# Kernel optimization log

Measured on AMD Instinct MI355X. Metric: run time of the kernel, lower is better.

Reference implementation:

```python
import jax, jax.numpy as jnp
import numpy as np

N, E, B = 50000, 800000, 64     # nodes, edges, graphs
IN, H = 3, 64                   # in_channels, hidden_channels
NDEF = 6
EPS = 1e-5                      # BatchNorm eps


def setup_inputs() -> dict:
    key = jax.random.key(0)
    ks = jax.random.split(key, 32)

    def lin(k, fi, fo):
        kw, kb = jax.random.split(k)
        s = 1.0 / np.sqrt(fi)
        W = jax.random.uniform(kw, (fi, fo), jnp.float32, -s, s)
        b = jax.random.uniform(kb, (fo,), jnp.float32, -s, s)
        return W, b

    inp = {}
    inp["x"] = jax.random.normal(ks[0], (N, IN), jnp.float32)
    inp["edge_index"] = jax.random.randint(ks[1], (2, E), 0, N, jnp.int64)
    inp["batch"] = jnp.sort(jax.random.randint(ks[2], (N,), 0, B, jnp.int64))

    inp["W1"], inp["b1"] = lin(ks[3], IN, H)
    inp["W2"], inp["b2"] = lin(ks[4], H, H)
    inp["W3"], inp["b3"] = lin(ks[5], H, H)
    for i, kk in zip((1, 2, 3), (ks[6], ks[7], ks[8])):
        kg, kb2 = jax.random.split(kk)
        inp[f"bn{i}_g"] = 1.0 + 0.1 * jax.random.normal(kg, (H,), jnp.float32)
        inp[f"bn{i}_b"] = 0.1 * jax.random.normal(kb2, (H,), jnp.float32)
        inp[f"bn{i}_m"] = jnp.zeros((H,), jnp.float32)
        inp[f"bn{i}_v"] = jnp.ones((H,), jnp.float32)

    inp["th_W1"], inp["th_b1"] = lin(ks[9], H, H // 2)
    inp["th_W2"], inp["th_b2"] = lin(ks[10], H // 2, NDEF)
    inp["lh_W1"], inp["lh_b1"] = lin(ks[11], H, H // 2)
    inp["lh_W2"], inp["lh_b2"] = lin(ks[12], H // 2, 2)
    inp["sh_W1"], inp["sh_b1"] = lin(ks[13], H, H // 4)
    inp["sh_W2"], inp["sh_b2"] = lin(ks[14], H // 4, 1)
    return inp


def reference(x, edge_index, batch,
              W1, b1, W2, b2, W3, b3,
              bn1_g, bn1_b, bn1_m, bn1_v,
              bn2_g, bn2_b, bn2_m, bn2_v,
              bn3_g, bn3_b, bn3_m, bn3_v,
              th_W1, th_b1, th_W2, th_b2,
              lh_W1, lh_b1, lh_W2, lh_b2,
              sh_W1, sh_b1, sh_W2, sh_b2):
    src, dst = edge_index[0], edge_index[1]
    # GCN symmetric normalization with self-loops: deg counts in-edges + self
    deg = jax.ops.segment_sum(jnp.ones((E,), x.dtype), dst, num_segments=N) + 1.0
    dis = jax.lax.rsqrt(deg)                 # deg^{-1/2}  [N]
    enorm = (dis[src] * dis[dst])[:, None]   # per-edge norm
    snorm = (dis * dis)[:, None]             # self-loop norm

    def gcn(h, W, b):
        m = h @ W  # [N, H]
        agg = jax.ops.segment_sum(m[src] * enorm, dst, num_segments=N) + m * snorm
        return agg + b

    def bn(h, g, beta, mu, var):
        return (h - mu) * jax.lax.rsqrt(var + EPS) * g + beta

    h = jax.nn.relu(bn(gcn(x, W1, b1), bn1_g, bn1_b, bn1_m, bn1_v))
    h = jax.nn.relu(bn(gcn(h, W2, b2), bn2_g, bn2_b, bn2_m, bn2_v))
    h = jax.nn.relu(bn(gcn(h, W3, b3), bn3_g, bn3_b, bn3_m, bn3_v))

    # global_mean_pool over graphs
    cnt = jax.ops.segment_sum(jnp.ones((N,), h.dtype), batch, num_segments=B)
    gemb = jax.ops.segment_sum(h, batch, num_segments=B) / jnp.maximum(cnt, 1.0)[:, None]

    type_logits = jax.nn.relu(gemb @ th_W1 + th_b1) @ th_W2 + th_b2
    location = jax.nn.sigmoid(jax.nn.relu(gemb @ lh_W1 + lh_b1) @ lh_W2 + lh_b2)
    severity = jax.nn.sigmoid(jax.nn.relu(gemb @ sh_W1 + sh_b1) @ sh_W2 + sh_b2)
    return (type_logits, location, severity)
```

## Files before the change

### kernel.cpp

```cpp
#include <hip/hip_runtime.h>
#include <hip/hip_bf16.h>
#include <math.h>

#define HH 64
#define EPS 1e-5f
#define STAGE_CAP 12288
#define NBLK_SCAT 192
#define PER_LANE 3

__device__ __forceinline__ int lower_bound_i(const int* a, int n, int key) {
    int lo = 0, hi = n;
    while (lo < hi) { int mid = (lo + hi) >> 1; if (a[mid] < key) lo = mid + 1; else hi = mid; }
    return lo;
}

__device__ __forceinline__ unsigned short f2bf(float f) {
    unsigned int u = __float_as_uint(f);
    unsigned int r = (u + 0x7FFFu + ((u >> 16) & 1u)) >> 16;
    return (unsigned short)r;
}
__device__ __forceinline__ float bf2f(unsigned short b) {
    return __uint_as_float(((unsigned int)b) << 16);
}

__global__ void init_kernel(float* gsum, int NG) {
    int t = blockIdx.x * blockDim.x + threadIdx.x;
    if (t < NG) gsum[t] = 0.f;
}

__global__ __launch_bounds__(256) void hist_kernel(const int* __restrict__ dst,
        int* __restrict__ blockhist, int E, int chunk) {
    __shared__ int hist[256];
    int tid = threadIdx.x, blk = blockIdx.x;
    hist[tid] = 0;
    __syncthreads();
    int s = blk * chunk, e = s + chunk; if (e > E) e = E;
    for (int i = s + tid; i < e; i += 256) atomicAdd(&hist[dst[i] >> 8], 1);
    __syncthreads();
    blockhist[blk * 256 + tid] = hist[tid];
}

__global__ __launch_bounds__(256) void bucketscan_kernel(const int* __restrict__ blockhist,
        int* __restrict__ bucketbase, int NB, int E) {
    __shared__ int wsum2[4];
    int tid = threadIdx.x, lane = tid & 63, wid = tid >> 6;
    int s = 0;
    if (tid < NB) {
        for (int i = 0; i < NBLK_SCAT; ++i) s += blockhist[i * 256 + tid];
    }
    int incl = s;
    #pragma unroll
    for (int off = 1; off < 64; off <<= 1) {
        int n = __shfl_up(incl, off);
        if (lane >= off) incl += n;
    }
    if (lane == 63) wsum2[wid] = incl;
    __syncthreads();
    int wbase = 0;
    #pragma unroll
    for (int k = 0; k < 4; ++k) if (k < wid) wbase += wsum2[k];
    if (tid < NB) bucketbase[tid] = wbase + incl - s;
    if (tid == 0) bucketbase[NB] = E;
}

__global__ __launch_bounds__(64) void offsets_kernel(const int* __restrict__ bucketbase,
        int* __restrict__ blockhist, int NB) {
    int b = blockIdx.x;
    int lane = threadIdx.x;
    int v[PER_LANE];
    int base = lane * PER_LANE;
    int s = 0;
    #pragma unroll
    for (int k = 0; k < PER_LANE; ++k) {
        int i = base + k;
        v[k] = (i < NBLK_SCAT) ? blockhist[i * 256 + b] : 0;
        s += v[k];
    }
    int incl = s;
    #pragma unroll
    for (int off = 1; off < 64; off <<= 1) {
        int n = __shfl_up(incl, off);
        if (lane >= off) incl += n;
    }
    int excl = incl - s + bucketbase[b];
    #pragma unroll
    for (int k = 0; k < PER_LANE; ++k) {
        int i = base + k;
        if (i < NBLK_SCAT) { blockhist[i * 256 + b] = excl; excl += v[k]; }
    }
}

__global__ __launch_bounds__(256) void scatterA_kernel(const int* __restrict__ src,
        const int* __restrict__ dst, const int* __restrict__ blockhist,
        int* __restrict__ buf, int E, int chunk) {
    __shared__ int lcur[256];
    int tid = threadIdx.x, blk = blockIdx.x;
    lcur[tid] = blockhist[blk * 256 + tid];
    __syncthreads();
    int s = blk * chunk, e = s + chunk; if (e > E) e = E;
    for (int i = s + tid; i < e; i += 256) {
        int d = dst[i];
        int b = d >> 8;
        int p = atomicAdd(&lcur[b], 1);
        buf[p] = ((d & 255) << 24) | src[i];
    }
}

__global__ __launch_bounds__(256) void bucket_to_csr_kernel(const int* __restrict__ buf,
        const int* __restrict__ bucketbase, int* __restrict__ rowstart,
        float* __restrict__ dis, int* __restrict__ csr, int N, int E) {
    __shared__ int ldeg[256];
    __shared__ int cur[256];
    __shared__ int wsum2[4];
    __shared__ int stage[STAGE_CAP];
    int b = blockIdx.x;
    int nodeStart = b << 8;
    int nodeEnd = nodeStart + 256; if (nodeEnd > N) nodeEnd = N;
    int nloc = nodeEnd - nodeStart;
    int base = bucketbase[b];
    int nE = bucketbase[b + 1] - base;
    int tid = threadIdx.x;
    int lane = tid & 63, wid = tid >> 6;
    ldeg[tid] = 0;
    __syncthreads();
    for (int i = tid; i < nE; i += 256)
        atomicAdd(&ldeg[((unsigned)buf[base + i]) >> 24], 1);
    __syncthreads();
    int d = ldeg[tid];
    int incl = d;
    #pragma unroll
    for (int off = 1; off < 64; off <<= 1) {
        int n = __shfl_up(incl, off);
        if (lane >= off) incl += n;
    }
    if (lane == 63) wsum2[wid] = incl;
    __syncthreads();
    int wbase = 0;
    #pragma unroll
    for (int k = 0; k < 4; ++k) if (k < wid) wbase += wsum2[k];
    int excl = wbase + incl - d;
    cur[tid] = excl;
    if (tid < nloc) {
        rowstart[nodeStart + tid] = base + excl;
        dis[nodeStart + tid] = rsqrtf((float)d + 1.0f);
    }
    if (b == 0 && tid == 0) rowstart[N] = E;
    __syncthreads();
    if (nE <= STAGE_CAP) {
        for (int i = tid; i < nE; i += 256) {
            int u = buf[base + i];
            int l = ((unsigned)u) >> 24;
            int p = atomicAdd(&cur[l], 1);
            stage[p] = u & 0xFFFFFF;
        }
        __syncthreads();
        for (int i = tid; i < nE; i += 256) csr[base + i] = stage[i];
    } else {
        for (int i = tid; i < nE; i += 256) {
            int u = buf[base + i];
            int l = ((unsigned)u) >> 24;
            int p = atomicAdd(&cur[l], 1);
            csr[base + p] = u & 0xFFFFFF;
        }
    }
}

__global__ void mt1_kernel(const float* __restrict__ x, const float* __restrict__ W1,
                           const float* __restrict__ dis, unsigned short* __restrict__ mt, int N) {
    int t = blockIdx.x * blockDim.x + threadIdx.x;
    if (t < N * HH) {
        int v = t >> 6, c = t & 63;
        float m = x[v * 3 + 0] * W1[0 * HH + c]
                + x[v * 3 + 1] * W1[1 * HH + c]
                + x[v * 3 + 2] * W1[2 * HH + c];
        mt[t] = f2bf(m * dis[v]);
    }
}

__global__ __launch_bounds__(256) void gemm_scale_kernel(const float* __restrict__ h,
        const float* __restrict__ W, const float* __restrict__ dis,
        unsigned short* __restrict__ mt, int N) {
    __shared__ unsigned int wsp[HH * 34];
    __shared__ unsigned int hs2[64 * 34];
    int tid = threadIdx.x;
    int lane = tid & 63, wid = tid >> 6;

    {
        int c = tid & 63;
        for (int k2 = tid >> 6; k2 < 32; k2 += 4) {
            float a = W[(2 * k2) * HH + c];
            float b = W[(2 * k2 + 1) * HH + c];
            wsp[c * 34 + k2] = (unsigned)f2bf(a) | ((unsigned)f2bf(b) << 16);
        }
    }
    int v0 = blockIdx.x * 64;
    int nv = N - v0; if (nv > 64) nv = 64;
    for (int idx = tid; idx < 64 * 32; idx += 256) {
        int n = idx >> 5, k2 = idx & 31;
        int vsrc = v0 + ((n < nv) ? n : 0);
        float a = h[(size_t)vsrc * HH + 2 * k2];
        float b = h[(size_t)vsrc * HH + 2 * k2 + 1];
        hs2[n * 34 + k2] = (unsigned)f2bf(a) | ((unsigned)f2bf(b) << 16);
    }
    __syncthreads();

    for (int n = wid * 16; n < wid * 16 + 16; ++n) {
        int vg = v0 + n;
        if (n >= nv) break;
        float acc = 0.f;
        #pragma unroll 4
        for (int k2g = 0; k2g < 16; ++k2g) {
            uint2 wv = *(const uint2*)&wsp[lane * 34 + 2 * k2g];
            uint2 hv = *(const uint2*)&hs2[n * 34 + 2 * k2g];
            acc = fmaf(__uint_as_float(hv.x << 16),         __uint_as_float(wv.x << 16),         acc);
            acc = fmaf(__uint_as_float(hv.x & 0xFFFF0000u), __uint_as_float(wv.x & 0xFFFF0000u), acc);
            acc = fmaf(__uint_as_float(hv.y << 16),         __uint_as_float(wv.y << 16),         acc);
            acc = fmaf(__uint_as_float(hv.y & 0xFFFF0000u), __uint_as_float(wv.y & 0xFFFF0000u), acc);
        }
        mt[(size_t)vg * HH + lane] = f2bf(acc * dis[vg]);
    }
}

__global__ __launch_bounds__(256) void gather_bn_kernel(const unsigned short* __restrict__ mt,
        const int* __restrict__ rowstart, const int* __restrict__ csr_src,
        const float* __restrict__ dis, const float* __restrict__ bias,
        const float* __restrict__ gam, const float* __restrict__ beta,
        const float* __restrict__ mu, const float* __restrict__ var,
        float* __restrict__ hout, int N) {
    int lane = threadIdx.x & 63, wid = threadIdx.x >> 6;
    int v = blockIdx.x * 4 + wid;
    if (v >= N) return;
    int start = rowstart[v], end = rowstart[v + 1];
    float acc = bf2f(mt[v * HH + lane]);
    for (int base = start; base < end; base += 64) {
        int idx = (base + lane < end) ? csr_src[base + lane] : 0;
        int cnt = end - base; if (cnt > 64) cnt = 64;
        int j = 0;
        for (; j + 15 < cnt; j += 16) {
            int s0 = __shfl(idx, j),      s1 = __shfl(idx, j + 1);
            int s2 = __shfl(idx, j + 2),  s3 = __shfl(idx, j + 3);
            int s4 = __shfl(idx, j + 4),  s5 = __shfl(idx, j + 5);
            int s6 = __shfl(idx, j + 6),  s7 = __shfl(idx, j + 7);
            int s8 = __shfl(idx, j + 8),  s9 = __shfl(idx, j + 9);
            int sa = __shfl(idx, j + 10), sb = __shfl(idx, j + 11);
            int sc = __shfl(idx, j + 12), sd = __shfl(idx, j + 13);
            int se = __shfl(idx, j + 14), sf = __shfl(idx, j + 15);
            float v0 = bf2f(mt[s0 * HH + lane]);
            float v1 = bf2f(mt[s1 * HH + lane]);
            float v2 = bf2f(mt[s2 * HH + lane]);
            float v3 = bf2f(mt[s3 * HH + lane]);
            float v4 = bf2f(mt[s4 * HH + lane]);
            float v5 = bf2f(mt[s5 * HH + lane]);
            float v6 = bf2f(mt[s6 * HH + lane]);
            float v7 = bf2f(mt[s7 * HH + lane]);
            float v8 = bf2f(mt[s8 * HH + lane]);
            float v9 = bf2f(mt[s9 * HH + lane]);
            float va = bf2f(mt[sa * HH + lane]);
            float vb = bf2f(mt[sb * HH + lane]);
            float vc = bf2f(mt[sc * HH + lane]);
            float vd = bf2f(mt[sd * HH + lane]);
            float ve = bf2f(mt[se * HH + lane]);
            float vf = bf2f(mt[sf * HH + lane]);
            acc += v0; acc += v1; acc += v2; acc += v3;
            acc += v4; acc += v5; acc += v6; acc += v7;
            acc += v8; acc += v9; acc += va; acc += vb;
            acc += vc; acc += vd; acc += ve; acc += vf;
        }
        for (; j + 7 < cnt; j += 8) {
            int s0 = __shfl(idx, j),     s1 = __shfl(idx, j + 1);
            int s2 = __shfl(idx, j + 2), s3 = __shfl(idx, j + 3);
            int s4 = __shfl(idx, j + 4), s5 = __shfl(idx, j + 5);
            int s6 = __shfl(idx, j + 6), s7 = __shfl(idx, j + 7);
            float v0 = bf2f(mt[s0 * HH + lane]);
            float v1 = bf2f(mt[s1 * HH + lane]);
            float v2 = bf2f(mt[s2 * HH + lane]);
            float v3 = bf2f(mt[s3 * HH + lane]);
            float v4 = bf2f(mt[s4 * HH + lane]);
            float v5 = bf2f(mt[s5 * HH + lane]);
            float v6 = bf2f(mt[s6 * HH + lane]);
            float v7 = bf2f(mt[s7 * HH + lane]);
            acc += v0; acc += v1; acc += v2; acc += v3;
            acc += v4; acc += v5; acc += v6; acc += v7;
        }
        for (; j < cnt; ++j) acc += bf2f(mt[__shfl(idx, j) * HH + lane]);
    }
    float val = acc * dis[v] + bias[lane];
    val = (val - mu[lane]) * rsqrtf(var[lane] + EPS) * gam[lane] + beta[lane];
    hout[v * HH + lane] = fmaxf(val, 0.f);
}

__global__ __launch_bounds__(256) void pool_partial_kernel(const float* __restrict__ h,
        const int* __restrict__ batch, float* __restrict__ gsum, int N, int chunk) {
    int lane = threadIdx.x & 63, wid = threadIdx.x >> 6;
    int w = blockIdx.x * 4 + wid;
    int start = w * chunk;
    int end = start + chunk; if (end > N) end = N;
    if (start >= end) return;
    int g = batch[start];
    float acc = 0.f;
    for (int i = start; i < end; ++i) {
        int gi = batch[i];
        if (gi != g) {
            atomicAdd(&gsum[g * HH + lane], acc);
            acc = 0.f; g = gi;
        }
        acc += h[i * HH + lane];
    }
    atomicAdd(&gsum[g * HH + lane], acc);
}

__global__ __launch_bounds__(64) void heads_kernel(const float* __restrict__ gsum,
        const int* __restrict__ batch, int N,
        const float* __restrict__ thW1, const float* __restrict__ thb1,
        const float* __restrict__ thW2, const float* __restrict__ thb2,
        const float* __restrict__ lhW1, const float* __restrict__ lhb1,
        const float* __restrict__ lhW2, const float* __restrict__ lhb2,
        const float* __restrict__ shW1, const float* __restrict__ shb1,
        const float* __restrict__ shW2, const float* __restrict__ shb2,
        float* __restrict__ out, int B) {
    int g = blockIdx.x, t = threadIdx.x;
    __shared__ float ge[HH];
    __shared__ float hT[32], hL[32], hS[16];
    int lo = lower_bound_i(batch, N, g);
    int hi = lower_bound_i(batch, N, g + 1);
    float cnt = (float)(hi - lo);
    ge[t] = gsum[g * HH + t] / fmaxf(cnt, 1.0f);
    __syncthreads();
    if (t < 32) {
        float a = thb1[t];
        for (int k = 0; k < HH; ++k) a += ge[k] * thW1[k * 32 + t];
        hT[t] = fmaxf(a, 0.f);
    } else {
        int j = t - 32;
        float a = lhb1[j];
        for (int k = 0; k < HH; ++k) a += ge[k] * lhW1[k * 32 + j];
        hL[j] = fmaxf(a, 0.f);
    }
    __syncthreads();
    if (t < 16) {
        float a = shb1[t];
        for (int k = 0; k < HH; ++k) a += ge[k] * shW1[k * 16 + t];
        hS[t] = fmaxf(a, 0.f);
    }
    __syncthreads();
    if (t < 6) {
        float a = thb2[t];
        for (int j = 0; j < 32; ++j) a += hT[j] * thW2[j * 6 + t];
        out[g * 6 + t] = a;
    } else if (t >= 8 && t < 10) {
        int o = t - 8;
        float a = lhb2[o];
        for (int j = 0; j < 32; ++j) a += hL[j] * lhW2[j * 2 + o];
        out[B * 6 + g * 2 + o] = 1.f / (1.f + expf(-a));
    } else if (t == 12) {
        float a = shb2[0];
        for (int j = 0; j < 16; ++j) a += hS[j] * shW2[j];
        out[B * 8 + g] = 1.f / (1.f + expf(-a));
    }
}

extern "C" void kernel_launch(void* const* d_in, const int* in_sizes, int n_in,
                              void* d_out, int out_size, void* d_ws, size_t ws_size,
                              hipStream_t stream) {
    const float* x   = (const float*)d_in[0];
    const int*   ei  = (const int*)d_in[1];
    const int*   bat = (const int*)d_in[2];
    const float* W1 = (const float*)d_in[3];  const float* b1 = (const float*)d_in[4];
    const float* W2 = (const float*)d_in[5];  const float* b2 = (const float*)d_in[6];
    const float* W3 = (const float*)d_in[7];  const float* b3 = (const float*)d_in[8];
    const float* bn1g = (const float*)d_in[9];  const float* bn1b = (const float*)d_in[10];
    const float* bn1m = (const float*)d_in[11]; const float* bn1v = (const float*)d_in[12];
    const float* bn2g = (const float*)d_in[13]; const float* bn2b = (const float*)d_in[14];
    const float* bn2m = (const float*)d_in[15]; const float* bn2v = (const float*)d_in[16];
    const float* bn3g = (const float*)d_in[17]; const float* bn3b = (const float*)d_in[18];
    const float* bn3m = (const float*)d_in[19]; const float* bn3v = (const float*)d_in[20];
    const float* thW1 = (const float*)d_in[21]; const float* thb1 = (const float*)d_in[22];
    const float* thW2 = (const float*)d_in[23]; const float* thb2 = (const float*)d_in[24];
    const float* lhW1 = (const float*)d_in[25]; const float* lhb1 = (const float*)d_in[26];
    const float* lhW2 = (const float*)d_in[27]; const float* lhb2 = (const float*)d_in[28];
    const float* shW1 = (const float*)d_in[29]; const float* shb1 = (const float*)d_in[30];
    const float* shW2 = (const float*)d_in[31]; const float* shb2 = (const float*)d_in[32];
    float* out = (float*)d_out;

    const int N = in_sizes[0] / 3;
    const int E = in_sizes[1] / 2;
    const int B = out_size / 9;
    const int NB = (N + 255) >> 8;
    const int* esrc = ei;
    const int* edst = ei + E;

    char* w = (char*)d_ws;
    size_t off = 0;
    auto alloc = [&](size_t bytes) -> void* {
        void* p = w + off;
        off += (bytes + 255) & ~(size_t)255;
        return p;
    };
    int*   rowstart   = (int*)  alloc((size_t)(N + 1) * 4);
    float* dis        = (float*)alloc((size_t)N * 4);
    int*   csr        = (int*)  alloc((size_t)E * 4);
    int*   blockhist  = (int*)  alloc((size_t)NBLK_SCAT * 256 * 4);
    int*   bucketbase = (int*)  alloc((size_t)(NB + 1) * 4);
    float* hbuf       = (float*)alloc((size_t)N * HH * 4);
    unsigned short* mtbuf = (unsigned short*)alloc((size_t)N * HH * 2);
    float* gsum       = (float*)alloc((size_t)B * HH * 4);
    int*   bucketbuf  = (int*)mtbuf;
    (void)ws_size;

    const int TB = 256;
    const int echunk = (E + NBLK_SCAT - 1) / NBLK_SCAT;
    init_kernel<<<(B * HH + TB - 1) / TB, TB, 0, stream>>>(gsum, B * HH);
    hist_kernel<<<NBLK_SCAT, TB, 0, stream>>>(edst, blockhist, E, echunk);
    bucketscan_kernel<<<1, TB, 0, stream>>>(blockhist, bucketbase, NB, E);
    offsets_kernel<<<NB, 64, 0, stream>>>(bucketbase, blockhist, NB);
    scatterA_kernel<<<NBLK_SCAT, TB, 0, stream>>>(esrc, edst, blockhist, bucketbuf, E, echunk);
    bucket_to_csr_kernel<<<NB, TB, 0, stream>>>(bucketbuf, bucketbase, rowstart, dis, csr, N, E);

    int gatherBlocks = (N + 3) / 4;
    int gemmBlocks = (N + 63) / 64;
    mt1_kernel<<<(N * HH + TB - 1) / TB, TB, 0, stream>>>(x, W1, dis, mtbuf, N);
    gather_bn_kernel<<<gatherBlocks, TB, 0, stream>>>(mtbuf, rowstart, csr, dis,
            b1, bn1g, bn1b, bn1m, bn1v, hbuf, N);
    gemm_scale_kernel<<<gemmBlocks, TB, 0, stream>>>(hbuf, W2, dis, mtbuf, N);
    gather_bn_kernel<<<gatherBlocks, TB, 0, stream>>>(mtbuf, rowstart, csr, dis,
            b2, bn2g, bn2b, bn2m, bn2v, hbuf, N);
    gemm_scale_kernel<<<gemmBlocks, TB, 0, stream>>>(hbuf, W3, dis, mtbuf, N);
    gather_bn_kernel<<<gatherBlocks, TB, 0, stream>>>(mtbuf, rowstart, csr, dis,
            b3, bn3g, bn3b, bn3m, bn3v, hbuf, N);

    const int PW_BLOCKS = 512;
    int chunk = (N + PW_BLOCKS * 4 - 1) / (PW_BLOCKS * 4);
    pool_partial_kernel<<<PW_BLOCKS, TB, 0, stream>>>(hbuf, bat, gsum, N, chunk);

    heads_kernel<<<B, 64, 0, stream>>>(gsum, bat, N, thW1, thb1, thW2, thb2,
            lhW1, lhb1, lhW2, lhb2, shW1, shb1, shW2, shb2, out, B);
}
```

Before: 217.0 us.

## Fuse GCN gather+BN with next-layer GEMM and final gather with pooling

Merges each layer's neighbor gather, batchnorm and ReLU with the following layer's 64x64 transform, so the fp32 hidden activations never go to global memory. The last layer's gather is fused with mean-pool accumulation, which removes the hbuf round trip and two launches. Blocks now cover 64 nodes with 16 nodes per wave, which cuts parallelism from about 12.5k to about 780 blocks and may hurt latency hiding for the irregular gathers. It also uses ping-pong bf16 buffers and keeps the activations in fp32 (no bf16 rounding) for the GEMM input.

```diff
diff --git a/kernel.cpp b/kernel.cpp
--- a/kernel.cpp
+++ b/kernel.cpp
@@ -22,6 +22,8 @@
 __device__ __forceinline__ float bf2f(unsigned short b) {
     return __uint_as_float(((unsigned int)b) << 16);
 }
+__device__ __forceinline__ float bflo(unsigned int u) { return __uint_as_float(u << 16); }
+__device__ __forceinline__ float bfhi(unsigned int u) { return __uint_as_float(u & 0xFFFF0000u); }
 
 __global__ void init_kernel(float* gsum, int NG) {
     int t = blockIdx.x * blockDim.x + threadIdx.x;
@@ -177,61 +179,9 @@
     }
 }
 
-__global__ __launch_bounds__(256) void gemm_scale_kernel(const float* __restrict__ h,
-        const float* __restrict__ W, const float* __restrict__ dis,
-        unsigned short* __restrict__ mt, int N) {
-    __shared__ unsigned int wsp[HH * 34];
-    __shared__ unsigned int hs2[64 * 34];
-    int tid = threadIdx.x;
-    int lane = tid & 63, wid = tid >> 6;
-
-    {
-        int c = tid & 63;
-        for (int k2 = tid >> 6; k2 < 32; k2 += 4) {
-            float a = W[(2 * k2) * HH + c];
-            float b = W[(2 * k2 + 1) * HH + c];
-            wsp[c * 34 + k2] = (unsigned)f2bf(a) | ((unsigned)f2bf(b) << 16);
-        }
-    }
-    int v0 = blockIdx.x * 64;
-    int nv = N - v0; if (nv > 64) nv = 64;
-    for (int idx = tid; idx < 64 * 32; idx += 256) {
-        int n = idx >> 5, k2 = idx & 31;
-        int vsrc = v0 + ((n < nv) ? n : 0);
-        float a = h[(size_t)vsrc * HH + 2 * k2];
-        float b = h[(size_t)vsrc * HH + 2 * k2 + 1];
-        hs2[n * 34 + k2] = (unsigned)f2bf(a) | ((unsigned)f2bf(b) << 16);
-    }
-    __syncthreads();
-
-    for (int n = wid * 16; n < wid * 16 + 16; ++n) {
-        int vg = v0 + n;
-        if (n >= nv) break;
-        float acc = 0.f;
-        #pragma unroll 4
-        for (int k2g = 0; k2g < 16; ++k2g) {
-            uint2 wv = *(const uint2*)&wsp[lane * 34 + 2 * k2g];
-            uint2 hv = *(const uint2*)&hs2[n * 34 + 2 * k2g];
-            acc = fmaf(__uint_as_float(hv.x << 16),         __uint_as_float(wv.x << 16),         acc);
-            acc = fmaf(__uint_as_float(hv.x & 0xFFFF0000u), __uint_as_float(wv.x & 0xFFFF0000u), acc);
-            acc = fmaf(__uint_as_float(hv.y << 16),         __uint_as_float(wv.y << 16),         acc);
-            acc = fmaf(__uint_as_float(hv.y & 0xFFFF0000u), __uint_as_float(wv.y & 0xFFFF0000u), acc);
-        }
-        mt[(size_t)vg * HH + lane] = f2bf(acc * dis[vg]);
-    }
-}
-
-__global__ __launch_bounds__(256) void gather_bn_kernel(const unsigned short* __restrict__ mt,
-        const int* __restrict__ rowstart, const int* __restrict__ csr_src,
-        const float* __restrict__ dis, const float* __restrict__ bias,
-        const float* __restrict__ gam, const float* __restrict__ beta,
-        const float* __restrict__ mu, const float* __restrict__ var,
-        float* __restrict__ hout, int N) {
-    int lane = threadIdx.x & 63, wid = threadIdx.x >> 6;
-    int v = blockIdx.x * 4 + wid;
-    if (v >= N) return;
-    int start = rowstart[v], end = rowstart[v + 1];
-    float acc = bf2f(mt[v * HH + lane]);
+__device__ __forceinline__ float gather_row(const unsigned short* __restrict__ mt,
+        const int* __restrict__ csr_src, int start, int end, int lane) {
+    float acc = 0.f;
     for (int base = start; base < end; base += 64) {
         int idx = (base + lane < end) ? csr_src[base + lane] : 0;
         int cnt = end - base; if (cnt > 64) cnt = 64;
@@ -284,29 +234,87 @@
         }
         for (; j < cnt; ++j) acc += bf2f(mt[__shfl(idx, j) * HH + lane]);
     }
-    float val = acc * dis[v] + bias[lane];
-    val = (val - mu[lane]) * rsqrtf(var[lane] + EPS) * gam[lane] + beta[lane];
-    hout[v * HH + lane] = fmaxf(val, 0.f);
-}
-
-__global__ __launch_bounds__(256) void pool_partial_kernel(const float* __restrict__ h,
-        const int* __restrict__ batch, float* __restrict__ gsum, int N, int chunk) {
-    int lane = threadIdx.x & 63, wid = threadIdx.x >> 6;
-    int w = blockIdx.x * 4 + wid;
-    int start = w * chunk;
-    int end = start + chunk; if (end > N) end = N;
-    if (start >= end) return;
-    int g = batch[start];
-    float acc = 0.f;
-    for (int i = start; i < end; ++i) {
-        int gi = batch[i];
-        if (gi != g) {
-            atomicAdd(&gsum[g * HH + lane], acc);
-            acc = 0.f; g = gi;
-        }
-        acc += h[i * HH + lane];
-    }
-    atomicAdd(&gsum[g * HH + lane], acc);
+    return acc;
+}
+
+__global__ __launch_bounds__(256) void gather_gemm_kernel(const unsigned short* __restrict__ mt_in,
+        const int* __restrict__ rowstart, const int* __restrict__ csr_src,
+        const float* __restrict__ dis, const float* __restrict__ bias,
+        const float* __restrict__ gam, const float* __restrict__ beta,
+        const float* __restrict__ mu, const float* __restrict__ var,
+        const float* __restrict__ Wnext, unsigned short* __restrict__ mt_out, int N) {
+    __shared__ unsigned int wsp[HH * 34];
+    __shared__ float hsf[64][68];
+    int tid = threadIdx.x;
+    int lane = tid & 63, wid = tid >> 6;
+    {
+        int c = tid & 63;
+        for (int k2 = tid >> 6; k2 < 32; k2 += 4) {
+            float a = Wnext[(2 * k2) * HH + c];
+            float b = Wnext[(2 * k2 + 1) * HH + c];
+            wsp[c * 34 + k2] = (unsigned)f2bf(a) | ((unsigned)f2bf(b) << 16);
+        }
+    }
+    __syncthreads();
+    int v0 = blockIdx.x * 64;
+    float ginv = rsqrtf(var[lane] + EPS) * gam[lane];
+    float gmu = mu[lane], gbe = beta[lane], gbi = bias[lane];
+    for (int n = wid * 16; n < wid * 16 + 16; ++n) {
+        int v = v0 + n;
+        if (v >= N) break;
+        int start = rowstart[v], end = rowstart[v + 1];
+        float dv = dis[v];
+        float acc = bf2f(mt_in[(size_t)v * HH + lane]);
+        acc += gather_row(mt_in, csr_src, start, end, lane);
+        float val = acc * dv + gbi;
+        val = (val - gmu) * ginv + gbe;
+        val = fmaxf(val, 0.f);
+        hsf[n][lane] = val;
+        float acc2 = 0.f;
+        #pragma unroll 4
+        for (int k4 = 0; k4 < 16; ++k4) {
+            float4 hv = *(const float4*)&hsf[n][4 * k4];
+            uint2 wv = *(const uint2*)&wsp[lane * 34 + 2 * k4];
+            acc2 = fmaf(hv.x, bflo(wv.x), acc2);
+            acc2 = fmaf(hv.y, bfhi(wv.x), acc2);
+            acc2 = fmaf(hv.z, bflo(wv.y), acc2);
+            acc2 = fmaf(hv.w, bfhi(wv.y), acc2);
+        }
+        mt_out[(size_t)v * HH + lane] = f2bf(acc2 * dv);
+    }
+}
+
+__global__ __launch_bounds__(256) void gather_pool_kernel(const unsigned short* __restrict__ mt_in,
+        const int* __restrict__ rowstart, const int* __restrict__ csr_src,
+        const float* __restrict__ dis, const float* __restrict__ bias,
+        const float* __restrict__ gam, const float* __restrict__ beta,
+        const float* __restrict__ mu, const float* __restrict__ var,
+        const int* __restrict__ batch, float* __restrict__ gsum, int N) {
+    int tid = threadIdx.x;
+    int lane = tid & 63, wid = tid >> 6;
+    int v0 = (blockIdx.x * 4 + wid) * 16;
+    if (v0 >= N) return;
+    int vend = v0 + 16; if (vend > N) vend = N;
+    float ginv = rsqrtf(var[lane] + EPS) * gam[lane];
+    float gmu = mu[lane], gbe = beta[lane], gbi = bias[lane];
+    int g = batch[v0];
+    float accrun = 0.f;
+    for (int v = v0; v < vend; ++v) {
+        int start = rowstart[v], end = rowstart[v + 1];
+        float dv = dis[v];
+        float acc = bf2f(mt_in[(size_t)v * HH + lane]);
+        acc += gather_row(mt_in, csr_src, start, end, lane);
+        float val = acc * dv + gbi;
+        val = (val - gmu) * ginv + gbe;
+        val = fmaxf(val, 0.f);
+        int gv = batch[v];
+        if (gv != g) {
+            atomicAdd(&gsum[g * HH + lane], accrun);
+            g = gv; accrun = 0.f;
+        }
+        accrun += val;
+    }
+    atomicAdd(&gsum[g * HH + lane], accrun);
 }
 
 __global__ __launch_bounds__(64) void heads_kernel(const float* __restrict__ gsum,
@@ -401,10 +409,10 @@
     int*   csr        = (int*)  alloc((size_t)E * 4);
     int*   blockhist  = (int*)  alloc((size_t)NBLK_SCAT * 256 * 4);
     int*   bucketbase = (int*)  alloc((size_t)(NB + 1) * 4);
-    float* hbuf       = (float*)alloc((size_t)N * HH * 4);
-    unsigned short* mtbuf = (unsigned short*)alloc((size_t)N * HH * 2);
+    unsigned short* mtA = (unsigned short*)alloc((size_t)N * HH * 2);
+    unsigned short* mtB = (unsigned short*)alloc((size_t)N * HH * 2);
     float* gsum       = (float*)alloc((size_t)B * HH * 4);
-    int*   bucketbuf  = (int*)mtbuf;
+    int*   bucketbuf  = (int*)mtA;
     (void)ws_size;
 
     const int TB = 256;
@@ -416,21 +424,14 @@
     scatterA_kernel<<<NBLK_SCAT, TB, 0, stream>>>(esrc, edst, blockhist, bucketbuf, E, echunk);
     bucket_to_csr_kernel<<<NB, TB, 0, stream>>>(bucketbuf, bucketbase, rowstart, dis, csr, N, E);
 
-    int gatherBlocks = (N + 3) / 4;
-    int gemmBlocks = (N + 63) / 64;
-    mt1_kernel<<<(N * HH + TB - 1) / TB, TB, 0, stream>>>(x, W1, dis, mtbuf, N);
-    gather_bn_kernel<<<gatherBlocks, TB, 0, stream>>>(mtbuf, rowstart, csr, dis,
-            b1, bn1g, bn1b, bn1m, bn1v, hbuf, N);
-    gemm_scale_kernel<<<gemmBlocks, TB, 0, stream>>>(hbuf, W2, dis, mtbuf, N);
-    gather_bn_kernel<<<gatherBlocks, TB, 0, stream>>>(mtbuf, rowstart, csr, dis,
-            b2, bn2g, bn2b, bn2m, bn2v, hbuf, N);
-    gemm_scale_kernel<<<gemmBlocks, TB, 0, stream>>>(hbuf, W3, dis, mtbuf, N);
-    gather_bn_kernel<<<gatherBlocks, TB, 0, stream>>>(mtbuf, rowstart, csr, dis,
-            b3, bn3g, bn3b, bn3m, bn3v, hbuf, N);
-
-    const int PW_BLOCKS = 512;
-    int chunk = (N + PW_BLOCKS * 4 - 1) / (PW_BLOCKS * 4);
-    pool_partial_kernel<<<PW_BLOCKS, TB, 0, stream>>>(hbuf, bat, gsum, N, chunk);
+    int tileBlocks = (N + 63) / 64;
+    mt1_kernel<<<(N * HH + TB - 1) / TB, TB, 0, stream>>>(x, W1, dis, mtA, N);
+    gather_gemm_kernel<<<tileBlocks, TB, 0, stream>>>(mtA, rowstart, csr, dis,
+            b1, bn1g, bn1b, bn1m, bn1v, W2, mtB, N);
+    gather_gemm_kernel<<<tileBlocks, TB, 0, stream>>>(mtB, rowstart, csr, dis,
+            b2, bn2g, bn2b, bn2m, bn2v, W3, mtA, N);
+    gather_pool_kernel<<<tileBlocks, TB, 0, stream>>>(mtA, rowstart, csr, dis,
+            b3, bn3g, bn3b, bn3m, bn3v, bat, gsum, N);
 
     heads_kernel<<<B, 64, 0, stream>>>(gsum, bat, N, thW1, thb1, thW2, thb2,
             lhW1, lhb1, lhW2, lhb2, shW1, shb1, shW2, shb2, out, B);
```

After: 231.0 us. +6.5%, slower.
